# Kernel tuning notes

Measured on AMD Instinct MI355X. Metric: run time of the kernel, lower is better.

Reference implementation:

```python
import jax, jax.numpy as jnp
import numpy as np
from jax import lax

# --- constants derived from init_kwargs ---
WAVE_RES = 4096          # round(sensor_diameter / pitch)
VALID_RES = 2048         # round(lens_diameter / pitch)
PITCH = 2e-6
SENSOR_D = WAVE_RES * PITCH
D1 = 0.05
D2 = 0.05
FOCAL = D1 * D2 / (D1 + D2)
WCROP = 728
LAMBDA = 5.32e-7
UP = 2                   # phase_upsample_factor
TWO_PI = 2.0 * np.pi


def _thomas(r):
    """Solve tridiagonal system with diag=4, off-diag=1 (Thomas algorithm)."""
    dt = r.dtype
    zero = jnp.zeros((), dt)

    def fwd(carry, ri):
        cp, dp = carry
        den = 4.0 - cp
        cpn = 1.0 / den
        dpn = (ri - dp) / den
        return (cpn, dpn), (cpn, dpn)

    _, (cps, dps) = lax.scan(fwd, (zero, zero), r)

    def bwd(x_next, cd):
        cp, dp = cd
        x = dp - cp * x_next
        return x, x

    _, xs = lax.scan(bwd, zero, (cps, dps), reverse=True)
    return xs


def _spline_eval(y, rq):
    """Natural cubic spline through (i, y[i]) on uniform grid, evaluated at rq.
    ind = searchsorted(arange(n), rq, 'left') - 1 == floor(rq) for this grid."""
    n = y.shape[0]
    rhs = 6.0 * (y[2:] - 2.0 * y[1:-1] + y[:-2])      # interior second-diff
    M = jnp.concatenate([jnp.zeros(1, y.dtype), _thomas(rhs), jnp.zeros(1, y.dtype)])
    ind = jnp.clip(jnp.floor(rq).astype(jnp.int32), 0, n - 2)
    t = rq - ind.astype(y.dtype)
    y0, y1 = y[ind], y[ind + 1]
    m0, m1 = M[ind], M[ind + 1]
    b = (y1 - y0) - (2.0 * m0 + m1) / 6.0
    return y0 + t * (b + t * (m0 / 2.0 + t * (m1 - m0) / 6.0))


def _phase_bias(optim_param):
    mp = jnp.repeat(optim_param, UP)                              # nearest upsample
    mp_log = jnp.concatenate([mp, jnp.zeros(VALID_RES // 2, mp.dtype)])  # len VALID_RES
    half = VALID_RES // 2
    coord = jnp.arange(half, dtype=jnp.float32) + 0.5
    r = jnp.sqrt(coord[:, None] ** 2 + coord[None, :] ** 2)       # [half, half]
    q = _spline_eval(mp_log, r)
    # copy_quadruple: mirror quadrant into full [VALID_RES, VALID_RES]
    row = jnp.concatenate([q[:, ::-1], q], axis=1)
    return jnp.concatenate([row[::-1, :], row], axis=0)


def _gen_psf(optim_param):
    k = TWO_PI / LAMBDA
    coords = PITCH * (jnp.arange(WAVE_RES, dtype=jnp.float32) - WAVE_RES // 2)
    DY, DX = jnp.meshgrid(coords, coords, indexing='ij')
    r2 = DX ** 2 + DY ** 2
    pad = (WAVE_RES - VALID_RES) // 2
    aperture = jnp.pad(jnp.ones((VALID_RES, VALID_RES), jnp.float32), pad)  # rect mask
    lens_phase = -(k * r2 / (2.0 * FOCAL))
    bias = jnp.pad(_phase_bias(optim_param), pad)
    fx = (jnp.arange(1, WAVE_RES + 1, dtype=jnp.float32) - WAVE_RES / 2) / SENSOR_D
    FY, FX = jnp.meshgrid(fx, fx, indexing='ij')
    w1 = jnp.sqrt(jnp.maximum((1.0 / LAMBDA) ** 2 - FX ** 2 - FY ** 2, 0.0))
    H_phase = TWO_PI * w1 * D2                                    # ASM transfer phase
    input_phase = k / (2.0 * D1) * r2                             # on-axis point source
    phase = jnp.mod(input_phase + lens_phase + bias, TWO_PI) * aperture
    field = aperture * lax.complex(jnp.cos(phase), jnp.sin(phase))
    spec = jnp.fft.fftshift(jnp.fft.fft2(field)) * lax.complex(jnp.cos(H_phase), jnp.sin(H_phase))
    psf_c = jnp.fft.ifft2(spec)
    psf = psf_c.real ** 2 + psf_c.imag ** 2
    c = WAVE_RES // 2
    s = c - WCROP // 2 + 1
    region = lax.dynamic_slice(psf, (s, s), (WCROP, WCROP))
    region = region / jnp.sum(region)
    return region[None, None]                                     # [1, 1, 728, 728]


def setup_inputs() -> dict:
    key = jax.random.key(0)
    optim_param = 0.1 * jax.random.normal(key, (VALID_RES // 2 // UP,), dtype=jnp.float32)
    return {"optim_param": optim_param}


def reference(optim_param):
    return _gen_psf(optim_param)
```

## Files before the change

kernel.cpp:

```cpp
#include <hip/hip_runtime.h>
#include <math.h>

constexpr double dPI     = 3.14159265358979323846;
constexpr double dLAMBDA = 5.32e-7;
constexpr double dK      = 2.0 * dPI / dLAMBDA;
constexpr double dD1     = 0.05;
constexpr double dD2     = 0.05;
constexpr double dFOCAL  = dD1 * dD2 / (dD1 + dD2);

constexpr float C1F         = (float)(dK / (2.0 * dD1));
constexpr float KFF         = (float)dK;
constexpr float TWO_FOCAL_F = (float)(2.0 * dFOCAL);
constexpr float TPF         = (float)(2.0 * dPI);
constexpr float INV_TPF     = (float)(1.0 / (2.0 * dPI));
constexpr float TPH         = (float)(2.0 * dPI);
constexpr float TPL         = (float)(2.0 * dPI - (double)TPH);
constexpr float SENSOR_DF   = (float)(4096.0 * 2e-6);
constexpr float ILAM2F      = (float)((1.0 / dLAMBDA) * (1.0 / dLAMBDA));
constexpr float D2F         = (float)dD2;
constexpr float PITCHF      = 2e-6f;
constexpr float SCALE       = 1.0f / 16777216.0f;

constexpr float TRI_R = -0.2679491924311227f;
constexpr float TRI_C = 0.2886751345948129f;

typedef float    v2f __attribute__((ext_vector_type(2)));
typedef _Float16 h2f __attribute__((ext_vector_type(2)));

__device__ __forceinline__ v2f mkv(float a, float b){ v2f r; r.x=a; r.y=b; return r; }
__device__ __forceinline__ h2f toh(v2f v){ h2f h; h.x=(_Float16)v.x; h.y=(_Float16)v.y; return h; }
__device__ __forceinline__ v2f tof(h2f h){ return mkv((float)h.x, (float)h.y); }

__device__ __forceinline__ v2f pkadd(v2f a, v2f b){
    v2f d;
    asm("v_pk_add_f32 %0, %1, %2" : "=v"(d) : "v"(a), "v"(b));
    return d;
}
__device__ __forceinline__ v2f pksub(v2f a, v2f b){
    v2f d;
    asm("v_pk_add_f32 %0, %1, %2 neg_lo:[0,1] neg_hi:[0,1]" : "=v"(d) : "v"(a), "v"(b));
    return d;
}
__device__ __forceinline__ v2f addmi(v2f a, v2f b){
    v2f d;
    asm("v_pk_add_f32 %0, %1, %2 op_sel:[0,1] op_sel_hi:[1,0] neg_hi:[0,1]"
        : "=v"(d) : "v"(a), "v"(b));
    return d;
}
__device__ __forceinline__ v2f addpi(v2f a, v2f b){
    v2f d;
    asm("v_pk_add_f32 %0, %1, %2 op_sel:[0,1] op_sel_hi:[1,0] neg_lo:[0,1]"
        : "=v"(d) : "v"(a), "v"(b));
    return d;
}
__device__ __forceinline__ v2f cmul(v2f a, v2f b){
    v2f t, d;
    asm("v_pk_mul_f32 %0, %1, %2 op_sel:[0,0] op_sel_hi:[0,1]"
        : "=v"(t) : "v"(a), "v"(b));
    asm("v_pk_fma_f32 %0, %1, %2, %3 op_sel:[1,1,0] op_sel_hi:[1,0,1] neg_lo:[1,0,0]"
        : "=v"(d) : "v"(a), "v"(b), "v"(t));
    return d;
}
__device__ __forceinline__ v2f cmulc(v2f a, v2f b){
    v2f t, d;
    asm("v_pk_mul_f32 %0, %1, %2 op_sel:[0,0] op_sel_hi:[0,1]"
        : "=v"(t) : "v"(a), "v"(b));
    asm("v_pk_fma_f32 %0, %1, %2, %3 op_sel:[1,1,0] op_sel_hi:[1,0,1] neg_hi:[0,0,1]"
        : "=v"(d) : "v"(a), "v"(b), "v"(t));
    return d;
}

__device__ __forceinline__ int digitrev12(int p){
    int r = __brev((unsigned)p) >> 20;
    return ((r & 0x555) << 1) | ((r >> 1) & 0x555);
}

__device__ __forceinline__ void bfly_fwd(v2f& A, v2f& B, v2f& C, v2f& D,
                                         v2f w1, v2f w2, v2f w3){
    v2f t0=pkadd(A,C), t1=pksub(A,C), t2=pkadd(B,D), t3=pksub(B,D);
    v2f y0=pkadd(t0,t2);
    v2f y1=addmi(t1,t3);
    v2f y2=pksub(t0,t2);
    v2f y3=addpi(t1,t3);
    A=y0; B=cmul(y1,w1); C=cmul(y2,w2); D=cmul(y3,w3);
}
__device__ __forceinline__ void bfly_fwd_nt(v2f& A, v2f& B, v2f& C, v2f& D){
    v2f t0=pkadd(A,C), t1=pksub(A,C), t2=pkadd(B,D), t3=pksub(B,D);
    A=pkadd(t0,t2);
    v2f y1=addmi(t1,t3);
    v2f y2=pksub(t0,t2);
    v2f y3=addpi(t1,t3);
    B=y1; C=y2; D=y3;
}
__device__ __forceinline__ void bfly_inv(v2f& A, v2f& B, v2f& C, v2f& D,
                                         v2f w1, v2f w2, v2f w3){
    v2f bb=cmulc(B,w1), cc=cmulc(C,w2), dd=cmulc(D,w3);
    v2f t0=pkadd(A,cc), t1=pksub(A,cc), t2=pkadd(bb,dd), t3=pksub(bb,dd);
    A=pkadd(t0,t2);
    B=addpi(t1,t3);
    C=pksub(t0,t2);
    D=addmi(t1,t3);
}
__device__ __forceinline__ void bfly_inv_nt(v2f& A, v2f& B, v2f& C, v2f& D){
    v2f t0=pkadd(A,C), t1=pksub(A,C), t2=pkadd(B,D), t3=pksub(B,D);
    A=pkadd(t0,t2);
    B=addpi(t1,t3);
    C=pksub(t0,t2);
    D=addmi(t1,t3);
}

template<bool ZAD>
__device__ __forceinline__ void front_fwd(v2f* r, int t,
        const v2f* __restrict__ tw1, const v2f* __restrict__ tw2,
        const v2f* __restrict__ tw3){
#pragma unroll
    for (int j = 0; j < 4; ++j){
        int m = t + 256*j;
        v2f w1 = tw1[m], w2 = tw2[m], w3 = tw3[m];
        v2f y0, y1, y2, y3;
        if (ZAD){
            v2f Bv = r[j+4], Cv = r[j+8];
            v2f nC = mkv(-Cv.x, -Cv.y);
            y0 = pkadd(Cv, Bv);
            y1 = addmi(nC, Bv);
            y2 = pksub(Cv, Bv);
            y3 = addpi(nC, Bv);
        } else {
            v2f Av=r[j], Bv=r[j+4], Cv=r[j+8], Dv=r[j+12];
            v2f t0=pkadd(Av,Cv), t1=pksub(Av,Cv), t2=pkadd(Bv,Dv), t3=pksub(Bv,Dv);
            y0=pkadd(t0,t2);
            y1=addmi(t1,t3);
            y2=pksub(t0,t2);
            y3=addpi(t1,t3);
        }
        r[j]=y0; r[j+4]=cmul(y1,w1); r[j+8]=cmul(y2,w2); r[j+12]=cmul(y3,w3);
    }
    v2f w1 = tw1[1024+t], w2 = tw2[1024+t], w3 = tw3[1024+t];
#pragma unroll
    for (int k = 0; k < 4; ++k)
        bfly_fwd(r[4*k], r[4*k+1], r[4*k+2], r[4*k+3], w1, w2, w3);
}
__device__ __forceinline__ void back_inv_crop(v2f* r, int t,
        const v2f* __restrict__ tw1, const v2f* __restrict__ tw2,
        const v2f* __restrict__ tw3,
        v2f& o6, v2f& o7, v2f& o8, v2f& o9){
    v2f w1 = tw1[1024+t], w2 = tw2[1024+t], w3 = tw3[1024+t];
#pragma unroll
    for (int k = 0; k < 4; ++k)
        bfly_inv(r[4*k], r[4*k+1], r[4*k+2], r[4*k+3], w1, w2, w3);
    {   v2f u1=tw1[t], u2=tw2[t], u3=tw3[t];
        v2f bb=cmulc(r[4],u1), cc=cmulc(r[8],u2), dd=cmulc(r[12],u3);
        o8 = pksub(pkadd(r[0],cc), pkadd(bb,dd));
    }
    {   v2f u1=tw1[t+256], u2=tw2[t+256], u3=tw3[t+256];
        v2f bb=cmulc(r[5],u1), cc=cmulc(r[9],u2), dd=cmulc(r[13],u3);
        o9 = pksub(pkadd(r[1],cc), pkadd(bb,dd));
    }
    {   v2f u1=tw1[t+512], u2=tw2[t+512], u3=tw3[t+512];
        v2f bb=cmulc(r[6],u1), cc=cmulc(r[10],u2), dd=cmulc(r[14],u3);
        v2f t1=pksub(r[2],cc), t3=pksub(bb,dd);
        o6 = addpi(t1,t3);
    }
    {   v2f u1=tw1[t+768], u2=tw2[t+768], u3=tw3[t+768];
        v2f bb=cmulc(r[7],u1), cc=cmulc(r[11],u2), dd=cmulc(r[15],u3);
        v2f t1=pksub(r[3],cc), t3=pksub(bb,dd);
        o7 = addpi(t1,t3);
    }
}
__device__ __forceinline__ void mid_fwd(v2f* r, int c,
        const v2f* __restrict__ tw1, const v2f* __restrict__ tw2,
        const v2f* __restrict__ tw3){
#pragma unroll
    for (int h = 0; h < 4; ++h){
        int idx = 1280 + 16*h + c;
        bfly_fwd(r[h], r[h+4], r[h+8], r[h+12], tw1[idx], tw2[idx], tw3[idx]);
    }
    v2f w1 = tw1[1344+c], w2 = tw2[1344+c], w3 = tw3[1344+c];
#pragma unroll
    for (int j = 0; j < 4; ++j)
        bfly_fwd(r[4*j], r[4*j+1], r[4*j+2], r[4*j+3], w1, w2, w3);
}
__device__ __forceinline__ void mid_inv(v2f* r, int c,
        const v2f* __restrict__ tw1, const v2f* __restrict__ tw2,
        const v2f* __restrict__ tw3){
    v2f w1 = tw1[1344+c], w2 = tw2[1344+c], w3 = tw3[1344+c];
#pragma unroll
    for (int j = 0; j < 4; ++j)
        bfly_inv(r[4*j], r[4*j+1], r[4*j+2], r[4*j+3], w1, w2, w3);
#pragma unroll
    for (int h = 0; h < 4; ++h){
        int idx = 1280 + 16*h + c;
        bfly_inv(r[h], r[h+4], r[h+8], r[h+12], tw1[idx], tw2[idx], tw3[idx]);
    }
}
#define C16F 0.9238795325112867f
#define S16F 0.3826834323650898f
#define C8F  0.7071067811865476f
__device__ __forceinline__ void tail_fwd(v2f* r){
    const v2f W1[4] = {mkv(1,0),mkv(C16F,-S16F),mkv(C8F,-C8F),mkv(S16F,-C16F)};
    const v2f W2[4] = {mkv(1,0),mkv(C8F,-C8F),mkv(0,-1),mkv(-C8F,-C8F)};
    const v2f W3[4] = {mkv(1,0),mkv(S16F,-C16F),mkv(-C8F,-C8F),mkv(-C16F,S16F)};
    bfly_fwd_nt(r[0], r[4], r[8], r[12]);
#pragma unroll
    for (int m = 1; m < 4; ++m)
        bfly_fwd(r[m], r[m+4], r[m+8], r[m+12], W1[m], W2[m], W3[m]);
#pragma unroll
    for (int h = 0; h < 4; ++h)
        bfly_fwd_nt(r[4*h], r[4*h+1], r[4*h+2], r[4*h+3]);
}
__device__ __forceinline__ void head_inv(v2f* r){
    const v2f W1[4] = {mkv(1,0),mkv(C16F,-S16F),mkv(C8F,-C8F),mkv(S16F,-C16F)};
    const v2f W2[4] = {mkv(1,0),mkv(C8F,-C8F),mkv(0,-1),mkv(-C8F,-C8F)};
    const v2f W3[4] = {mkv(1,0),mkv(S16F,-C16F),mkv(-C8F,-C8F),mkv(-C16F,S16F)};
#pragma unroll
    for (int h = 0; h < 4; ++h)
        bfly_inv_nt(r[4*h], r[4*h+1], r[4*h+2], r[4*h+3]);
    bfly_inv_nt(r[0], r[4], r[8], r[12]);
#pragma unroll
    for (int m = 1; m < 4; ++m)
        bfly_inv(r[m], r[m+4], r[m+8], r[m+12], W1[m], W2[m], W3[m]);
}

__device__ __forceinline__ void x_strided_to_mid(v2f* r, v2f* lds, int t){
    int tsw = t ^ (t >> 4);
#pragma unroll
    for (int q = 0; q < 16; ++q) lds[256*q + tsw] = r[q];
    __syncthreads();
    int Bq = (t >> 4) * 256, c = t & 15;
#pragma unroll
    for (int g = 0; g < 16; ++g) r[g] = lds[Bq + 16*g + (c ^ g)];
}
__device__ __forceinline__ void x_mid_to_contig(v2f* r, v2f* lds, int t){
    int Bq = (t >> 4) * 256, c = t & 15;
#pragma unroll
    for (int g = 0; g < 16; ++g) lds[Bq + 16*g + (c ^ g)] = r[g];
    __syncthreads();
    int tl = t & 15, base = 16*t;
#pragma unroll
    for (int g = 0; g < 16; ++g) r[g] = lds[base + (g ^ tl)];
}
__device__ __forceinline__ void x_contig_to_mid(v2f* r, v2f* lds, int t){
    int tl = t & 15, base = 16*t;
#pragma unroll
    for (int g = 0; g < 16; ++g) lds[base + (g ^ tl)] = r[g];
    __syncthreads();
    int Bq = (t >> 4) * 256, c = t & 15;
#pragma unroll
    for (int g = 0; g < 16; ++g) r[g] = lds[Bq + 16*g + (c ^ g)];
}
__device__ __forceinline__ void x_mid_to_strided(v2f* r, v2f* lds, int t){
    int Bq = (t >> 4) * 256, c = t & 15;
#pragma unroll
    for (int g = 0; g < 16; ++g) lds[Bq + 16*g + (c ^ g)] = r[g];
    __syncthreads();
    int tsw = t ^ (t >> 4);
#pragma unroll
    for (int q = 0; q < 16; ++q) r[q] = lds[256*q + tsw];
}

__global__ __launch_bounds__(256) void k_setup(const float* __restrict__ p,
        float* __restrict__ Mv, v2f* __restrict__ tw1,
        v2f* __restrict__ tw2, v2f* __restrict__ tw3){
    int bid = blockIdx.x;
    int t = threadIdx.x;
    if (bid >= 8){
        int idx = (bid - 8) * 256 + t;
        if (idx >= 1360) return;
        int m, L;
        if (idx < 1024)      { m = idx;        L = 4096; }
        else if (idx < 1280) { m = idx - 1024; L = 1024; }
        else if (idx < 1344) { m = idx - 1280; L = 256;  }
        else                 { m = idx - 1344; L = 64;   }
        double ang = -2.0 * dPI * (double)m / (double)L;
        double s1, c1, s2, c2v, s3, c3;
        sincos(ang, &s1, &c1);
        sincos(2.0*ang, &s2, &c2v);
        sincos(3.0*ang, &s3, &c3);
        tw1[idx] = mkv((float)c1,  (float)s1);
        tw2[idx] = mkv((float)c2v, (float)s2);
        tw3[idx] = mkv((float)c3,  (float)s3);
        return;
    }
    __shared__ float sY[328];
    int B0 = bid * 256;
    for (int k = t; k < 324; k += 256){
        int jg = B0 - 32 + k;
        sY[k] = (jg >= 0 && jg < 1024) ? p[jg >> 1] : 0.0f;
    }
    __syncthreads();
    int i = B0 + t;
    if (i >= 2046) return;
    auto rhs = [&](int j) -> float {
        if (j < 0 || j >= 2046) return 0.0f;
        int l = j - B0 + 32;
        return 6.0f * (sY[l+2] - 2.0f*sY[l+1] + sY[l]);
    };
    float x = TRI_C * rhs(i);
    float wd = TRI_C;
    for (int d = 1; d <= 32; ++d){
        wd *= TRI_R;
        x += wd * (rhs(i-d) + rhs(i+d));
    }
    if (i < 48){
        float cA = 0.0f, wj = TRI_C;
        for (int j = 0; j < 32; ++j){ wj *= TRI_R; cA += wj * rhs(j); }
        float rp = 1.0f;
        for (int k = 0; k <= i; ++k) rp *= TRI_R;
        x -= cA * rp;
    }
    if (i >= 1998){
        float cB = 0.0f, wj = TRI_C;
        for (int j = 0; j < 32; ++j){ wj *= TRI_R; cB += wj * rhs(2045 - j); }
        float rp = 1.0f;
        for (int k = 0; k < 2046 - i; ++k) rp *= TRI_R;
        x -= cB * rp;
    }
    Mv[i+1] = x;
    if (i == 0)    Mv[0]    = 0.0f;
    if (i == 2045) Mv[2047] = 0.0f;
}

__global__ __launch_bounds__(256) void k_pass1(const float* __restrict__ p,
        const float* __restrict__ Mv,
        const v2f* __restrict__ tw1, const v2f* __restrict__ tw2,
        const v2f* __restrict__ tw3, h2f* __restrict__ F1){
    __shared__ v2f lds[4096];
    float* ldsf = (float*)lds;
    int t = threadIdx.x;
    int row = blockIdx.x;
    v2f r[16];
    for (int j = t; j < 512; j += 256)  ldsf[j] = p[j];
    for (int j = t; j < 2048; j += 256) ldsf[512 + j] = Mv[j];
    __syncthreads();
    int y = 1024 + row;
    int iy = row;
    int a = (iy < 1024) ? (1023 - iy) : (iy - 1024);
    float fy = PITCHF * (float)(y - 2048);
    float cy2 = fy * fy;
    float af = (float)a + 0.5f;
#pragma unroll
    for (int q = 4; q < 12; ++q){
        int x = t + 256*q;
        int ix = x - 1024;
        int b = (ix < 1024) ? (1023 - ix) : (ix - 1024);
        float bf = (float)b + 0.5f;
        float rq = sqrtf(af*af + bf*bf);
        int ind = (int)rq; if (ind > 2046) ind = 2046;
        float tt = rq - (float)ind;
        float y0v = (ind < 1024) ? ldsf[ind >> 1] : 0.0f;
        float y1v = (ind + 1 < 1024) ? ldsf[(ind + 1) >> 1] : 0.0f;
        float m0 = ldsf[512 + ind], m1 = ldsf[512 + ind + 1];
        float bb = (y1v - y0v) - (2.0f*m0 + m1) / 6.0f;
        float bias = y0v + tt*(bb + tt*(m0/2.0f + tt*(m1-m0)/6.0f));
        float fx = PITCHF * (float)(x - 2048);
        float r2 = fx*fx + cy2;
        float ip = C1F * r2;
        float lp = -((KFF * r2) / TWO_FOCAL_F);
        float sp = ip + lp + bias;
        float fv = sp * INV_TPF;
        float fr = fv - floorf(fv);
        float sn = __builtin_amdgcn_sinf(fr);
        float cs = __builtin_amdgcn_cosf(fr);
        r[q] = mkv(cs, sn);
    }
    __syncthreads();
    front_fwd<true>(r, t, tw1, tw2, tw3);
    x_strided_to_mid(r, lds, t);
    mid_fwd(r, t & 15, tw1, tw2, tw3);
    x_mid_to_contig(r, lds, t);
    tail_fwd(r);
    size_t base = (size_t)row * 4096;
#pragma unroll
    for (int g = 0; g < 16; ++g)
        F1[base + 256*g + t] = toh(r[g]);
}

__global__ __launch_bounds__(256) void k_transpose_h(const unsigned* __restrict__ in,
                                                     unsigned* __restrict__ out,
                                                     int H, int W){
    __shared__ unsigned tile[64][65];
    int bx = blockIdx.x * 64, by = blockIdx.y * 64;
    int tx = threadIdx.x, ty = threadIdx.y;
#pragma unroll
    for (int k = 0; k < 4; ++k){
        int rr = by + ty + 16*k;
        int cc = bx + 4*tx;
        if (cc + 3 < W){
            uint4 v = *(const uint4*)&in[(size_t)rr * W + cc];
            tile[ty+16*k][4*tx+0] = v.x;
            tile[ty+16*k][4*tx+1] = v.y;
            tile[ty+16*k][4*tx+2] = v.z;
            tile[ty+16*k][4*tx+3] = v.w;
        } else {
#pragma unroll
            for (int j = 0; j < 4; ++j)
                if (cc + j < W) tile[ty+16*k][4*tx+j] = in[(size_t)rr * W + cc + j];
        }
    }
    __syncthreads();
#pragma unroll
    for (int k = 0; k < 4; ++k){
        int rr = bx + ty + 16*k;
        int cc = by + 4*tx;
        if (rr < W){
            uint4 v;
            v.x = tile[4*tx+0][ty+16*k];
            v.y = tile[4*tx+1][ty+16*k];
            v.z = tile[4*tx+2][ty+16*k];
            v.w = tile[4*tx+3][ty+16*k];
            *(uint4*)&out[(size_t)rr * H + cc] = v;
        }
    }
}

__global__ __launch_bounds__(256, 8) void k_pass2(const h2f* __restrict__ F1T,
        const v2f* __restrict__ tw1, const v2f* __restrict__ tw2,
        const v2f* __restrict__ tw3, h2f* __restrict__ GT){
    __shared__ v2f lds[4096];
    int t = threadIdx.x;
    int cp = blockIdx.x;
    v2f r[16];
    size_t base = (size_t)cp * 2048;
#pragma unroll
    for (int q = 4; q < 12; ++q)
        r[q] = tof(F1T[base + t + 256*(q-4)]);
    front_fwd<true>(r, t, tw1, tw2, tw3);
    x_strided_to_mid(r, lds, t);
    mid_fwd(r, t & 15, tw1, tw2, tw3);
    x_mid_to_contig(r, lds, t);
    tail_fwd(r);
    int pcol = ((cp & 255) << 4) | (cp >> 8);
    int kx = digitrev12(pcol);
    int kxs = (kx + 2048) & 4095;
    float fxv = ((float)(kxs + 1) - 2048.0f) / SENSOR_DF;
    float fx2 = fxv * fxv;
    int rt = __brev((unsigned)t) >> 24;
    rt = ((rt & 0x55) << 1) | ((rt >> 1) & 0x55);
#pragma unroll
    for (int g = 0; g < 16; ++g){
        const int rg = ((g & 3) << 2) | (g >> 2);
        int ky = rg * 256 + rt;
        int kys = (ky + 2048) & 4095;
        float fyv = ((float)(kys + 1) - 2048.0f) / SENSOR_DF;
        float arg = ILAM2F - fx2 - fyv*fyv;
        arg = fmaxf(arg, 0.0f);
        float w1v = sqrtf(arg);
        float Hp = (TPF * w1v) * D2F;
        float v  = Hp * INV_TPF;
        float nn = rintf(v);
        float rr = fmaf(nn, -TPH, Hp);
        rr       = fmaf(nn, -TPL, rr);
        float rev = rr * INV_TPF;
        float sn = __builtin_amdgcn_sinf(rev);
        float cs = __builtin_amdgcn_cosf(rev);
        r[g] = cmul(r[g], mkv(cs * SCALE, sn * SCALE));
    }
    head_inv(r);
    x_contig_to_mid(r, lds, t);
    mid_inv(r, t & 15, tw1, tw2, tw3);
    x_mid_to_strided(r, lds, t);
    v2f o6, o7, o8, o9;
    back_inv_crop(r, t, tw1, tw2, tw3, o6, o7, o8, o9);
    size_t ob = (size_t)cp * 728;
    if (t >= 149) GT[ob + t - 149] = toh(o6);
    GT[ob + t + 107] = toh(o7);
    GT[ob + t + 363] = toh(o8);
    if (t < 109)  GT[ob + t + 619] = toh(o9);
}

__global__ __launch_bounds__(256, 8) void k_pass3(const h2f* __restrict__ G,
        float* __restrict__ out, float* __restrict__ partials,
        const v2f* __restrict__ tw1, const v2f* __restrict__ tw2,
        const v2f* __restrict__ tw3){
    __shared__ v2f lds[4096];
    int t = threadIdx.x;
    int row = blockIdx.x;
    v2f r[16];
    size_t base = (size_t)row * 4096;
#pragma unroll
    for (int g = 0; g < 16; ++g)
        r[g] = tof(G[base + 256*g + t]);
    head_inv(r);
    x_contig_to_mid(r, lds, t);
    mid_inv(r, t & 15, tw1, tw2, tw3);
    x_mid_to_strided(r, lds, t);
    v2f o6, o7, o8, o9;
    back_inv_crop(r, t, tw1, tw2, tw3, o6, o7, o8, o9);
    float lsum = 0.0f;
    size_t ob = (size_t)row * 728;
    if (t >= 149){ float I = o6.x*o6.x + o6.y*o6.y; out[ob + t - 149] = I; lsum += I; }
    { float I = o7.x*o7.x + o7.y*o7.y; out[ob + t + 107] = I; lsum += I; }
    { float I = o8.x*o8.x + o8.y*o8.y; out[ob + t + 363] = I; lsum += I; }
    if (t < 109){ float I = o9.x*o9.x + o9.y*o9.y; out[ob + t + 619] = I; lsum += I; }
    __syncthreads();
    float* red = (float*)lds;
    red[t] = lsum;
    __syncthreads();
    for (int k2 = 128; k2 > 0; k2 >>= 1){
        if (t < k2) red[t] += red[t + k2];
        __syncthreads();
    }
    if (t == 0) partials[row] = red[0];
}

__global__ __launch_bounds__(256) void k_norm(float* __restrict__ out,
                                              const float* __restrict__ partials,
                                              int n){
    __shared__ float red[256];
    int t = threadIdx.x;
    float s = 0.0f;
    for (int i = t; i < 728; i += 256) s += partials[i];
    red[t] = s;
    __syncthreads();
    for (int k = 128; k > 0; k >>= 1){
        if (t < k) red[t] += red[t + k];
        __syncthreads();
    }
    float total = red[0];
    int i = blockIdx.x * 256 + t;
    if (i < n) out[i] = out[i] / total;
}

extern "C" void kernel_launch(void* const* d_in, const int* in_sizes, int n_in,
                              void* d_out, int out_size, void* d_ws, size_t ws_size,
                              hipStream_t stream) {
    const float* p   = (const float*)d_in[0];
    float*       out = (float*)d_out;
    char*        ws  = (char*)d_ws;

    float* Mv       = (float*)(ws + 8192);
    float* partials = (float*)(ws + 16384);
    v2f*   tw1      = (v2f*)(ws + 24576);
    v2f*   tw2      = (v2f*)(ws + 40960);
    v2f*   tw3      = (v2f*)(ws + 57344);

    const size_t BIG = (size_t)64 * 1024 * 1024;
    h2f* F1  = (h2f*)(ws + (1 << 20));
    h2f* F1T = (h2f*)(ws + (1 << 20) + BIG);
    h2f* GT  = F1;
    h2f* G   = F1T;

    k_setup<<<14, 256, 0, stream>>>(p, Mv, tw1, tw2, tw3);
    k_pass1<<<2048, 256, 0, stream>>>(p, Mv, tw1, tw2, tw3, F1);
    k_transpose_h<<<dim3(64, 32), dim3(16, 16), 0, stream>>>((const unsigned*)F1, (unsigned*)F1T, 2048, 4096);
    k_pass2<<<4096, 256, 0, stream>>>(F1T, tw1, tw2, tw3, GT);
    k_transpose_h<<<dim3(12, 64), dim3(16, 16), 0, stream>>>((const unsigned*)GT, (unsigned*)G, 4096, 728);
    k_pass3<<<728, 256, 0, stream>>>(G, out, partials, tw1, tw2, tw3);
    int n = out_size;
    k_norm<<<(n + 255) / 256, 256, 0, stream>>>(out, partials, n);
}
```

Baseline: 114.0 us.

## Process two FFT columns per block in pass2 to share twiddles and syncs

k_pass2 now handles two columns per 256-thread block, holding both in registers and interleaving their butterflies so each twiddle load serves two columns. Grid size halves and launch bounds drop the occupancy hint of 8. The aim is to cut repeated twiddle loads and raise instruction-level parallelism. In exchange, register pressure roughly doubles, which lowers occupancy, and the LDS exchanges for the two columns run one after the other with extra barriers.

```diff
diff --git a/kernel.cpp b/kernel.cpp
--- a/kernel.cpp
+++ b/kernel.cpp
@@ -221,6 +221,116 @@
         bfly_inv(r[m], r[m+4], r[m+8], r[m+12], W1[m], W2[m], W3[m]);
 }
 
+template<bool ZAD>
+__device__ __forceinline__ void front_fwd2(v2f* ra, v2f* rb, int t,
+        const v2f* __restrict__ tw1, const v2f* __restrict__ tw2,
+        const v2f* __restrict__ tw3){
+#pragma unroll
+    for (int j = 0; j < 4; ++j){
+        int m = t + 256*j;
+        v2f w1 = tw1[m], w2 = tw2[m], w3 = tw3[m];
+#pragma unroll
+        for (int s = 0; s < 2; ++s){
+            v2f* r = s ? rb : ra;
+            v2f y0, y1, y2, y3;
+            if (ZAD){
+                v2f Bv = r[j+4], Cv = r[j+8];
+                v2f nC = mkv(-Cv.x, -Cv.y);
+                y0 = pkadd(Cv, Bv);
+                y1 = addmi(nC, Bv);
+                y2 = pksub(Cv, Bv);
+                y3 = addpi(nC, Bv);
+            } else {
+                v2f Av=r[j], Bv=r[j+4], Cv=r[j+8], Dv=r[j+12];
+                v2f t0=pkadd(Av,Cv), t1=pksub(Av,Cv), t2=pkadd(Bv,Dv), t3=pksub(Bv,Dv);
+                y0=pkadd(t0,t2);
+                y1=addmi(t1,t3);
+                y2=pksub(t0,t2);
+                y3=addpi(t1,t3);
+            }
+            r[j]=y0; r[j+4]=cmul(y1,w1); r[j+8]=cmul(y2,w2); r[j+12]=cmul(y3,w3);
+        }
+    }
+    v2f w1 = tw1[1024+t], w2 = tw2[1024+t], w3 = tw3[1024+t];
+#pragma unroll
+    for (int k = 0; k < 4; ++k){
+        bfly_fwd(ra[4*k], ra[4*k+1], ra[4*k+2], ra[4*k+3], w1, w2, w3);
+        bfly_fwd(rb[4*k], rb[4*k+1], rb[4*k+2], rb[4*k+3], w1, w2, w3);
+    }
+}
+__device__ __forceinline__ void mid_fwd2(v2f* ra, v2f* rb, int c,
+        const v2f* __restrict__ tw1, const v2f* __restrict__ tw2,
+        const v2f* __restrict__ tw3){
+#pragma unroll
+    for (int h = 0; h < 4; ++h){
+        int idx = 1280 + 16*h + c;
+        v2f u1=tw1[idx], u2=tw2[idx], u3=tw3[idx];
+        bfly_fwd(ra[h], ra[h+4], ra[h+8], ra[h+12], u1, u2, u3);
+        bfly_fwd(rb[h], rb[h+4], rb[h+8], rb[h+12], u1, u2, u3);
+    }
+    v2f w1 = tw1[1344+c], w2 = tw2[1344+c], w3 = tw3[1344+c];
+#pragma unroll
+    for (int j = 0; j < 4; ++j){
+        bfly_fwd(ra[4*j], ra[4*j+1], ra[4*j+2], ra[4*j+3], w1, w2, w3);
+        bfly_fwd(rb[4*j], rb[4*j+1], rb[4*j+2], rb[4*j+3], w1, w2, w3);
+    }
+}
+__device__ __forceinline__ void mid_inv2(v2f* ra, v2f* rb, int c,
+        const v2f* __restrict__ tw1, const v2f* __restrict__ tw2,
+        const v2f* __restrict__ tw3){
+    v2f w1 = tw1[1344+c], w2 = tw2[1344+c], w3 = tw3[1344+c];
+#pragma unroll
+    for (int j = 0; j < 4; ++j){
+        bfly_inv(ra[4*j], ra[4*j+1], ra[4*j+2], ra[4*j+3], w1, w2, w3);
+        bfly_inv(rb[4*j], rb[4*j+1], rb[4*j+2], rb[4*j+3], w1, w2, w3);
+    }
+#pragma unroll
+    for (int h = 0; h < 4; ++h){
+        int idx = 1280 + 16*h + c;
+        v2f u1=tw1[idx], u2=tw2[idx], u3=tw3[idx];
+        bfly_inv(ra[h], ra[h+4], ra[h+8], ra[h+12], u1, u2, u3);
+        bfly_inv(rb[h], rb[h+4], rb[h+8], rb[h+12], u1, u2, u3);
+    }
+}
+__device__ __forceinline__ void back_inv_crop2(v2f* ra, v2f* rb, int t,
+        const v2f* __restrict__ tw1, const v2f* __restrict__ tw2,
+        const v2f* __restrict__ tw3, v2f* oa, v2f* ob){
+    v2f w1 = tw1[1024+t], w2 = tw2[1024+t], w3 = tw3[1024+t];
+#pragma unroll
+    for (int k = 0; k < 4; ++k){
+        bfly_inv(ra[4*k], ra[4*k+1], ra[4*k+2], ra[4*k+3], w1, w2, w3);
+        bfly_inv(rb[4*k], rb[4*k+1], rb[4*k+2], rb[4*k+3], w1, w2, w3);
+    }
+    {   v2f u1=tw1[t], u2=tw2[t], u3=tw3[t];
+        v2f bb=cmulc(ra[4],u1), cc=cmulc(ra[8],u2), dd=cmulc(ra[12],u3);
+        oa[2] = pksub(pkadd(ra[0],cc), pkadd(bb,dd));
+        bb=cmulc(rb[4],u1); cc=cmulc(rb[8],u2); dd=cmulc(rb[12],u3);
+        ob[2] = pksub(pkadd(rb[0],cc), pkadd(bb,dd));
+    }
+    {   v2f u1=tw1[t+256], u2=tw2[t+256], u3=tw3[t+256];
+        v2f bb=cmulc(ra[5],u1), cc=cmulc(ra[9],u2), dd=cmulc(ra[13],u3);
+        oa[3] = pksub(pkadd(ra[1],cc), pkadd(bb,dd));
+        bb=cmulc(rb[5],u1); cc=cmulc(rb[9],u2); dd=cmulc(rb[13],u3);
+        ob[3] = pksub(pkadd(rb[1],cc), pkadd(bb,dd));
+    }
+    {   v2f u1=tw1[t+512], u2=tw2[t+512], u3=tw3[t+512];
+        v2f bb=cmulc(ra[6],u1), cc=cmulc(ra[10],u2), dd=cmulc(ra[14],u3);
+        v2f t1=pksub(ra[2],cc), t3=pksub(bb,dd);
+        oa[0] = addpi(t1,t3);
+        bb=cmulc(rb[6],u1); cc=cmulc(rb[10],u2); dd=cmulc(rb[14],u3);
+        t1=pksub(rb[2],cc); t3=pksub(bb,dd);
+        ob[0] = addpi(t1,t3);
+    }
+    {   v2f u1=tw1[t+768], u2=tw2[t+768], u3=tw3[t+768];
+        v2f bb=cmulc(ra[7],u1), cc=cmulc(ra[11],u2), dd=cmulc(ra[15],u3);
+        v2f t1=pksub(ra[3],cc), t3=pksub(bb,dd);
+        oa[1] = addpi(t1,t3);
+        bb=cmulc(rb[7],u1); cc=cmulc(rb[11],u2); dd=cmulc(rb[15],u3);
+        t1=pksub(rb[3],cc); t3=pksub(bb,dd);
+        ob[1] = addpi(t1,t3);
+    }
+}
+
 __device__ __forceinline__ void x_strided_to_mid(v2f* r, v2f* lds, int t){
     int tsw = t ^ (t >> 4);
 #pragma unroll
@@ -256,6 +366,66 @@
     int tsw = t ^ (t >> 4);
 #pragma unroll
     for (int q = 0; q < 16; ++q) r[q] = lds[256*q + tsw];
+}
+__device__ __forceinline__ void x2_strided_to_mid(v2f* ra, v2f* rb, v2f* lds, int t){
+    int tsw = t ^ (t >> 4);
+    int Bq = (t >> 4) * 256, c = t & 15;
+#pragma unroll
+    for (int q = 0; q < 16; ++q) lds[256*q + tsw] = ra[q];
+    __syncthreads();
+#pragma unroll
+    for (int g = 0; g < 16; ++g) ra[g] = lds[Bq + 16*g + (c ^ g)];
+    __syncthreads();
+#pragma unroll
+    for (int q = 0; q < 16; ++q) lds[256*q + tsw] = rb[q];
+    __syncthreads();
+#pragma unroll
+    for (int g = 0; g < 16; ++g) rb[g] = lds[Bq + 16*g + (c ^ g)];
+}
+__device__ __forceinline__ void x2_mid_to_contig(v2f* ra, v2f* rb, v2f* lds, int t){
+    int Bq = (t >> 4) * 256, c = t & 15;
+    int tl = t & 15, base = 16*t;
+#pragma unroll
+    for (int g = 0; g < 16; ++g) lds[Bq + 16*g + (c ^ g)] = ra[g];
+    __syncthreads();
+#pragma unroll
+    for (int g = 0; g < 16; ++g) ra[g] = lds[base + (g ^ tl)];
+    __syncthreads();
+#pragma unroll
+    for (int g = 0; g < 16; ++g) lds[Bq + 16*g + (c ^ g)] = rb[g];
+    __syncthreads();
+#pragma unroll
+    for (int g = 0; g < 16; ++g) rb[g] = lds[base + (g ^ tl)];
+}
+__device__ __forceinline__ void x2_contig_to_mid(v2f* ra, v2f* rb, v2f* lds, int t){
+    int tl = t & 15, base = 16*t;
+    int Bq = (t >> 4) * 256, c = t & 15;
+#pragma unroll
+    for (int g = 0; g < 16; ++g) lds[base + (g ^ tl)] = ra[g];
+    __syncthreads();
+#pragma unroll
+    for (int g = 0; g < 16; ++g) ra[g] = lds[Bq + 16*g + (c ^ g)];
+    __syncthreads();
+#pragma unroll
+    for (int g = 0; g < 16; ++g) lds[base + (g ^ tl)] = rb[g];
+    __syncthreads();
+#pragma unroll
+    for (int g = 0; g < 16; ++g) rb[g] = lds[Bq + 16*g + (c ^ g)];
+}
+__device__ __forceinline__ void x2_mid_to_strided(v2f* ra, v2f* rb, v2f* lds, int t){
+    int Bq = (t >> 4) * 256, c = t & 15;
+    int tsw = t ^ (t >> 4);
+#pragma unroll
+    for (int g = 0; g < 16; ++g) lds[Bq + 16*g + (c ^ g)] = ra[g];
+    __syncthreads();
+#pragma unroll
+    for (int q = 0; q < 16; ++q) ra[q] = lds[256*q + tsw];
+    __syncthreads();
+#pragma unroll
+    for (int g = 0; g < 16; ++g) lds[Bq + 16*g + (c ^ g)] = rb[g];
+    __syncthreads();
+#pragma unroll
+    for (int q = 0; q < 16; ++q) rb[q] = lds[256*q + tsw];
 }
 
 __global__ __launch_bounds__(256) void k_setup(const float* __restrict__ p,
@@ -413,27 +583,33 @@
     }
 }
 
-__global__ __launch_bounds__(256, 8) void k_pass2(const h2f* __restrict__ F1T,
+__global__ __launch_bounds__(256) void k_pass2(const h2f* __restrict__ F1T,
         const v2f* __restrict__ tw1, const v2f* __restrict__ tw2,
         const v2f* __restrict__ tw3, h2f* __restrict__ GT){
     __shared__ v2f lds[4096];
     int t = threadIdx.x;
-    int cp = blockIdx.x;
-    v2f r[16];
-    size_t base = (size_t)cp * 2048;
-#pragma unroll
-    for (int q = 4; q < 12; ++q)
-        r[q] = tof(F1T[base + t + 256*(q-4)]);
-    front_fwd<true>(r, t, tw1, tw2, tw3);
-    x_strided_to_mid(r, lds, t);
-    mid_fwd(r, t & 15, tw1, tw2, tw3);
-    x_mid_to_contig(r, lds, t);
-    tail_fwd(r);
-    int pcol = ((cp & 255) << 4) | (cp >> 8);
-    int kx = digitrev12(pcol);
-    int kxs = (kx + 2048) & 4095;
-    float fxv = ((float)(kxs + 1) - 2048.0f) / SENSOR_DF;
-    float fx2 = fxv * fxv;
+    int cp0 = 2 * blockIdx.x, cp1 = cp0 + 1;
+    v2f ra[16], rb[16];
+    size_t base0 = (size_t)cp0 * 2048;
+    size_t base1 = (size_t)cp1 * 2048;
+#pragma unroll
+    for (int q = 4; q < 12; ++q){
+        ra[q] = tof(F1T[base0 + t + 256*(q-4)]);
+        rb[q] = tof(F1T[base1 + t + 256*(q-4)]);
+    }
+    front_fwd2<true>(ra, rb, t, tw1, tw2, tw3);
+    x2_strided_to_mid(ra, rb, lds, t);
+    mid_fwd2(ra, rb, t & 15, tw1, tw2, tw3);
+    x2_mid_to_contig(ra, rb, lds, t);
+    tail_fwd(ra); tail_fwd(rb);
+    int pcol0 = ((cp0 & 255) << 4) | (cp0 >> 8);
+    int pcol1 = ((cp1 & 255) << 4) | (cp1 >> 8);
+    int kxs0 = (digitrev12(pcol0) + 2048) & 4095;
+    int kxs1 = (digitrev12(pcol1) + 2048) & 4095;
+    float fxv0 = ((float)(kxs0 + 1) - 2048.0f) / SENSOR_DF;
+    float fxv1 = ((float)(kxs1 + 1) - 2048.0f) / SENSOR_DF;
+    float fx20 = fxv0 * fxv0;
+    float fx21 = fxv1 * fxv1;
     int rt = __brev((unsigned)t) >> 24;
     rt = ((rt & 0x55) << 1) | ((rt >> 1) & 0x55);
 #pragma unroll
@@ -442,30 +618,42 @@
         int ky = rg * 256 + rt;
         int kys = (ky + 2048) & 4095;
         float fyv = ((float)(kys + 1) - 2048.0f) / SENSOR_DF;
-        float arg = ILAM2F - fx2 - fyv*fyv;
-        arg = fmaxf(arg, 0.0f);
-        float w1v = sqrtf(arg);
-        float Hp = (TPF * w1v) * D2F;
-        float v  = Hp * INV_TPF;
-        float nn = rintf(v);
-        float rr = fmaf(nn, -TPH, Hp);
-        rr       = fmaf(nn, -TPL, rr);
-        float rev = rr * INV_TPF;
-        float sn = __builtin_amdgcn_sinf(rev);
-        float cs = __builtin_amdgcn_cosf(rev);
-        r[g] = cmul(r[g], mkv(cs * SCALE, sn * SCALE));
-    }
-    head_inv(r);
-    x_contig_to_mid(r, lds, t);
-    mid_inv(r, t & 15, tw1, tw2, tw3);
-    x_mid_to_strided(r, lds, t);
-    v2f o6, o7, o8, o9;
-    back_inv_crop(r, t, tw1, tw2, tw3, o6, o7, o8, o9);
-    size_t ob = (size_t)cp * 728;
-    if (t >= 149) GT[ob + t - 149] = toh(o6);
-    GT[ob + t + 107] = toh(o7);
-    GT[ob + t + 363] = toh(o8);
-    if (t < 109)  GT[ob + t + 619] = toh(o9);
+        float fy2 = fyv * fyv;
+        {   float arg = fmaxf(ILAM2F - fx20 - fy2, 0.0f);
+            float Hp = (TPF * sqrtf(arg)) * D2F;
+            float v  = Hp * INV_TPF;
+            float nn = rintf(v);
+            float rr2 = fmaf(nn, -TPH, Hp);
+            rr2       = fmaf(nn, -TPL, rr2);
+            float rev = rr2 * INV_TPF;
+            float sn = __builtin_amdgcn_sinf(rev);
+            float cs = __builtin_amdgcn_cosf(rev);
+            ra[g] = cmul(ra[g], mkv(cs * SCALE, sn * SCALE));
+        }
+        {   float arg = fmaxf(ILAM2F - fx21 - fy2, 0.0f);
+            float Hp = (TPF * sqrtf(arg)) * D2F;
+            float v  = Hp * INV_TPF;
+            float nn = rintf(v);
+            float rr2 = fmaf(nn, -TPH, Hp);
+            rr2       = fmaf(nn, -TPL, rr2);
+            float rev = rr2 * INV_TPF;
+            float sn = __builtin_amdgcn_sinf(rev);
+            float cs = __builtin_amdgcn_cosf(rev);
+            rb[g] = cmul(rb[g], mkv(cs * SCALE, sn * SCALE));
+        }
+    }
+    head_inv(ra); head_inv(rb);
+    x2_contig_to_mid(ra, rb, lds, t);
+    mid_inv2(ra, rb, t & 15, tw1, tw2, tw3);
+    x2_mid_to_strided(ra, rb, lds, t);
+    v2f oa[4], ob[4];
+    back_inv_crop2(ra, rb, t, tw1, tw2, tw3, oa, ob);
+    size_t ob0 = (size_t)cp0 * 728;
+    size_t ob1 = (size_t)cp1 * 728;
+    if (t >= 149){ GT[ob0 + t - 149] = toh(oa[0]); GT[ob1 + t - 149] = toh(ob[0]); }
+    GT[ob0 + t + 107] = toh(oa[1]); GT[ob1 + t + 107] = toh(ob[1]);
+    GT[ob0 + t + 363] = toh(oa[2]); GT[ob1 + t + 363] = toh(ob[2]);
+    if (t < 109){ GT[ob0 + t + 619] = toh(oa[3]); GT[ob1 + t + 619] = toh(ob[3]); }
 }
 
 __global__ __launch_bounds__(256, 8) void k_pass3(const h2f* __restrict__ G,
@@ -543,7 +731,7 @@
     k_setup<<<14, 256, 0, stream>>>(p, Mv, tw1, tw2, tw3);
     k_pass1<<<2048, 256, 0, stream>>>(p, Mv, tw1, tw2, tw3, F1);
     k_transpose_h<<<dim3(64, 32), dim3(16, 16), 0, stream>>>((const unsigned*)F1, (unsigned*)F1T, 2048, 4096);
-    k_pass2<<<4096, 256, 0, stream>>>(F1T, tw1, tw2, tw3, GT);
+    k_pass2<<<2048, 256, 0, stream>>>(F1T, tw1, tw2, tw3, GT);
     k_transpose_h<<<dim3(12, 64), dim3(16, 16), 0, stream>>>((const unsigned*)GT, (unsigned*)G, 4096, 728);
     k_pass3<<<728, 256, 0, stream>>>(G, out, partials, tw1, tw2, tw3);
     int n = out_size;
```

Result: faster. 110.8 us (median of 2 runs) (-2.8%).
